# Optimization experiments

Hardware: AMD Instinct MI355X
Metric: run time of the kernel (lower is better)

The kernel has to match this reference:

```python
import jax, jax.numpy as jnp
import numpy as np

B, N, C = 2, 2048, 1024
H = 16
D = C // H
HID = 4 * C
EPS = 1e-5


def layernorm(x, g, b):
    mu = jnp.mean(x, axis=-1, keepdims=True)
    var = jnp.var(x, axis=-1, keepdims=True)
    return (x - mu) * jax.lax.rsqrt(var + EPS) * g + b


def setup_inputs() -> dict:
    key = jax.random.key(0)
    ks = jax.random.split(key, 8)
    s = lambda fan_in: 1.0 / np.sqrt(fan_in)
    return {
        "x": jax.random.normal(ks[0], (B, N, C), dtype=jnp.float32),
        "ln1_g": jnp.ones((C,), jnp.float32),
        "ln1_b": jnp.zeros((C,), jnp.float32),
        "w_qkv": jax.random.normal(ks[1], (C, 3 * C), jnp.float32) * s(C),
        "w_proj": jax.random.normal(ks[2], (C, C), jnp.float32) * s(C),
        "b_proj": jnp.zeros((C,), jnp.float32),
        "ln2_g": jnp.ones((C,), jnp.float32),
        "ln2_b": jnp.zeros((C,), jnp.float32),
        "w_fc1": jax.random.normal(ks[3], (C, HID), jnp.float32) * s(C),
        "b_fc1": jnp.zeros((HID,), jnp.float32),
        "w_fc2": jax.random.normal(ks[4], (HID, C), jnp.float32) * s(HID),
        "b_fc2": jnp.zeros((C,), jnp.float32),
        "metadata": 0,
        "thw_shape": 2048,
    }


def reference(x, ln1_g, ln1_b, w_qkv, w_proj, b_proj, ln2_g, ln2_b,
              w_fc1, b_fc1, w_fc2, b_fc2, metadata, thw_shape):
    scale = 1.0 / np.sqrt(D)
    # --- attention branch (pre-norm) ---
    xn = layernorm(x, ln1_g, ln1_b)
    qkv = (xn @ w_qkv).reshape(B, N, 3, H, D)
    q = jnp.transpose(qkv[:, :, 0], (0, 2, 1, 3))  # [B,H,N,D]
    k = jnp.transpose(qkv[:, :, 1], (0, 2, 1, 3))
    v = jnp.transpose(qkv[:, :, 2], (0, 2, 1, 3))
    attn = jax.nn.softmax(jnp.einsum('bhnd,bhmd->bhnm', q, k) * scale, axis=-1)
    o = jnp.einsum('bhnm,bhmd->bhnd', attn, v)
    o = jnp.transpose(o, (0, 2, 1, 3)).reshape(B, N, C)
    x = x + (o @ w_proj + b_proj)
    # --- MLP branch (pre-norm) ---
    xn2 = layernorm(x, ln2_g, ln2_b)
    h = jax.nn.gelu(xn2 @ w_fc1 + b_fc1, approximate=False)  # torch GELU = exact erf
    x = x + (h @ w_fc2 + b_fc2)
    return x
```

## Files before the change

kernel.cpp:

```cpp
#include <hip/hip_runtime.h>

#define B_   2
#define N_   2048
#define C_   1024
#define H_   16
#define D_   64
#define HID_ 4096
#define M_   (B_ * N_)

typedef __attribute__((ext_vector_type(8))) short bf16x8;
typedef __attribute__((ext_vector_type(4))) short short4v;
typedef __attribute__((ext_vector_type(4))) float f32x4;

__device__ __forceinline__ unsigned short f2bf(float f) {
  unsigned int u = __builtin_bit_cast(unsigned int, f);
  u += 0x7fffu + ((u >> 16) & 1u);
  return (unsigned short)(u >> 16);
}

__device__ __forceinline__ void gl2lds16(const void* g, void* l) {
  __builtin_amdgcn_global_load_lds(
      (const __attribute__((address_space(1))) unsigned int*)g,
      (__attribute__((address_space(3))) unsigned int*)l, 16, 0, 0);
}

__global__ __launch_bounds__(256) void ln_kernel(const float* __restrict__ x,
                                                 const float* __restrict__ g,
                                                 const float* __restrict__ bta,
                                                 unsigned short* __restrict__ out) {
  int row  = blockIdx.x * 4 + (threadIdx.x >> 6);
  int lane = threadIdx.x & 63;
  const float* xr = x + (size_t)row * C_;
  float4 v[4];
  float s1 = 0.f, s2 = 0.f;
#pragma unroll
  for (int j = 0; j < 4; j++) {
    v[j] = *(const float4*)(xr + j * 256 + lane * 4);
    s1 += v[j].x + v[j].y + v[j].z + v[j].w;
    s2 += v[j].x * v[j].x + v[j].y * v[j].y + v[j].z * v[j].z + v[j].w * v[j].w;
  }
#pragma unroll
  for (int m = 1; m < 64; m <<= 1) { s1 += __shfl_xor(s1, m); s2 += __shfl_xor(s2, m); }
  float mu  = s1 * (1.0f / C_);
  float var = s2 * (1.0f / C_) - mu * mu;
  float rs  = rsqrtf(var + 1e-5f);
#pragma unroll
  for (int j = 0; j < 4; j++) {
    const float4 gv = *(const float4*)(g + j * 256 + lane * 4);
    const float4 bv = *(const float4*)(bta + j * 256 + lane * 4);
    ushort4 o;
    o.x = f2bf((v[j].x - mu) * rs * gv.x + bv.x);
    o.y = f2bf((v[j].y - mu) * rs * gv.y + bv.y);
    o.z = f2bf((v[j].z - mu) * rs * gv.z + bv.z);
    o.w = f2bf((v[j].w - mu) * rs * gv.w + bv.w);
    *(ushort4*)(out + (size_t)row * C_ + j * 256 + lane * 4) = o;
  }
}

__global__ __launch_bounds__(256) void wtrans_kernel(const float* __restrict__ W,
                                                     unsigned short* __restrict__ Wt,
                                                     int K, int N) {
  __shared__ float t[32][33];
  int n0 = blockIdx.x * 32, k0 = blockIdx.y * 32;
  int tx = threadIdx.x, ty = threadIdx.y;
#pragma unroll
  for (int j = 0; j < 4; j++)
    t[ty + j * 8][tx] = W[(size_t)(k0 + ty + j * 8) * N + n0 + tx];
  __syncthreads();
#pragma unroll
  for (int j = 0; j < 4; j++)
    Wt[(size_t)(n0 + ty + j * 8) * K + k0 + tx] = f2bf(t[tx][ty + j * 8]);
}

__global__ __launch_bounds__(256) void vtrans_kernel(const unsigned short* __restrict__ v,
                                                     unsigned short* __restrict__ vt) {
  __shared__ unsigned short t[32][33];
  int bh = blockIdx.z;
  int n0 = blockIdx.x * 32, d0 = blockIdx.y * 32;
  const unsigned short* src = v + (size_t)bh * N_ * D_;
  unsigned short* dst = vt + (size_t)bh * D_ * N_;
  int tx = threadIdx.x, ty = threadIdx.y;
#pragma unroll
  for (int j = 0; j < 4; j++)
    t[ty + j * 8][tx] = src[(size_t)(n0 + ty + j * 8) * D_ + d0 + tx];
  __syncthreads();
#pragma unroll
  for (int j = 0; j < 4; j++)
    dst[(size_t)(d0 + ty + j * 8) * N_ + n0 + tx] = t[tx][ty + j * 8];
}

template <int MODE, int BN>
__global__ __launch_bounds__(256) void gemm_kernel(
    const unsigned short* __restrict__ A,
    const unsigned short* __restrict__ Wt,
    const float* __restrict__ bias,
    const float* __restrict__ resid,
    float* __restrict__ outf,
    unsigned short* __restrict__ outb0,
    unsigned short* __restrict__ outb1,
    unsigned short* __restrict__ outb2,
    int M, int N, int K) {
  constexpr int MT = (BN == 128) ? 4 : 2;
  __shared__ __align__(16) short As[128][64];
  __shared__ __align__(16) short Bs[BN][64];
  int tid = threadIdx.x;
  int w = tid >> 6, lane = tid & 63, r = lane & 15, quad = lane >> 4;
  int rowbase = (BN == 128) ? (w >> 1) * 64 : w * 32;
  int colbase = (BN == 128) ? (w & 1) * 64 : 0;
  int bM = blockIdx.y * 128, bN = blockIdx.x * BN;

  int srow   = (w << 3) + (lane >> 3);
  int schunk = (lane & 7) ^ ((lane >> 3) & 7);
  const unsigned short* aP = A  + (size_t)(bM + srow) * K + schunk * 8;
  const unsigned short* bP = Wt + (size_t)(bN + srow) * K + schunk * 8;

  int pc0 = (quad ^ (r & 7)) * 8;

  f32x4 acc[MT][4];
#pragma unroll
  for (int i = 0; i < MT; i++)
#pragma unroll
    for (int j = 0; j < 4; j++) acc[i][j] = f32x4{0.f, 0.f, 0.f, 0.f};

  for (int k0 = 0; k0 < K; k0 += 64) {
    __syncthreads();
#pragma unroll
    for (int p = 0; p < 4; p++)
      gl2lds16(aP + (size_t)(p * 32) * K + k0, &As[p * 32 + (w << 3)][0]);
#pragma unroll
    for (int p = 0; p < BN / 32; p++)
      gl2lds16(bP + (size_t)(p * 32) * K + k0, &Bs[p * 32 + (w << 3)][0]);
    __syncthreads();
#pragma unroll
    for (int kh = 0; kh < 2; kh++) {
      int pc = pc0 ^ (kh * 32);
      bf16x8 af[MT], bfr[4];
#pragma unroll
      for (int mt = 0; mt < MT; mt++)
        af[mt] = *(const bf16x8*)&As[rowbase + mt * 16 + r][pc];
#pragma unroll
      for (int nt = 0; nt < 4; nt++)
        bfr[nt] = *(const bf16x8*)&Bs[colbase + nt * 16 + r][pc];
#pragma unroll
      for (int mt = 0; mt < MT; mt++)
#pragma unroll
        for (int nt = 0; nt < 4; nt++)
          acc[mt][nt] = __builtin_amdgcn_mfma_f32_16x16x32_bf16(af[mt], bfr[nt], acc[mt][nt], 0, 0, 0);
    }
  }

#pragma unroll
  for (int mt = 0; mt < MT; mt++) {
#pragma unroll
    for (int nt = 0; nt < 4; nt++) {
#pragma unroll
      for (int i = 0; i < 4; i++) {
        int gm = bM + rowbase + mt * 16 + quad * 4 + i;
        int gn = bN + colbase + nt * 16 + r;
        float val = acc[mt][nt][i];
        if (MODE == 0) {
          int s = gn >> 10, c = gn & 1023;
          int hh = c >> 6, d = c & 63;
          int b = gm >> 11, n = gm & 2047;
          size_t di = ((size_t)(b * H_ + hh) * N_ + n) * D_ + d;
          unsigned short bvv = f2bf(s == 0 ? val * 0.125f : val);
          (s == 0 ? outb0 : (s == 1 ? outb1 : outb2))[di] = bvv;
        } else if (MODE == 1) {
          outf[(size_t)gm * N + gn] = val + bias[gn] + resid[(size_t)gm * N + gn];
        } else {
          float t = val + bias[gn];
          float gl = 0.5f * t * (1.0f + erff(t * 0.70710678118f));
          outb0[(size_t)gm * N + gn] = f2bf(gl);
        }
      }
    }
  }
}

template <int MODE>
__global__ __launch_bounds__(512, 2) void gemm256_kernel(
    const unsigned short* __restrict__ A,
    const unsigned short* __restrict__ Wt,
    const float* __restrict__ bias,
    float* __restrict__ outf,
    const float* __restrict__ resid,
    unsigned short* __restrict__ outb0,
    unsigned short* __restrict__ outb1,
    unsigned short* __restrict__ outb2,
    int M, int N, int K) {
  __shared__ __align__(16) short As[2][256][64];
  __shared__ __align__(16) short Bs[2][256][64];
  const int tid = threadIdx.x;
  const int w = tid >> 6, lane = tid & 63, r = lane & 15, quad = lane >> 4;
  const int wr = w >> 2, wc = w & 3;
  const int bN = blockIdx.x * 256, bM = blockIdx.y * 256;

  const int srow   = (w << 3) + (lane >> 3);
  const int schunk = (lane & 7) ^ ((lane >> 3) & 7);
  const unsigned short* aSrc = A  + (size_t)(bM + srow) * K + schunk * 8;
  const unsigned short* bSrc = Wt + (size_t)(bN + srow) * K + schunk * 8;
  const int wrow = w << 3;

  const int ntiles = K >> 6;
  const int tmask  = ntiles - 1;

#define STAGE_H(t, h)                                                            \
  do {                                                                           \
    int b_ = (t) & 1, tt_ = (t) & tmask;                                         \
    if ((h) < 2) {                                                               \
      const unsigned short* p_ = aSrc + (size_t)((h) * 128) * K + tt_ * 64;      \
      gl2lds16(p_, &As[b_][(h) * 128 + wrow][0]);                                \
      gl2lds16(p_ + (size_t)64 * K, &As[b_][(h) * 128 + 64 + wrow][0]);          \
    } else {                                                                     \
      const unsigned short* p_ = bSrc + (size_t)(((h) - 2) * 128) * K + tt_ * 64;\
      gl2lds16(p_, &Bs[b_][((h) - 2) * 128 + wrow][0]);                          \
      gl2lds16(p_ + (size_t)64 * K, &Bs[b_][((h) - 2) * 128 + 64 + wrow][0]);    \
    }                                                                            \
  } while (0)

  f32x4 acc[8][4];
#pragma unroll
  for (int i = 0; i < 8; i++)
#pragma unroll
    for (int j = 0; j < 4; j++) acc[i][j] = f32x4{0.f, 0.f, 0.f, 0.f};

  bf16x8 af[4][2];
  bf16x8 bfr[4][2];

#define RD_A(b, msub)                                                            \
  {                                                                              \
    _Pragma("unroll") for (int mt_ = 0; mt_ < 4; mt_++)                          \
      _Pragma("unroll") for (int ks_ = 0; ks_ < 2; ks_++)                        \
        af[mt_][ks_] = *(const bf16x8*)&As[b][wr * 128 + (msub) * 64 + mt_ * 16 + r] \
                                          [((ks_ * 4 + quad) ^ (r & 7)) * 8];    \
  }
#define RD_B(b, nh)                                                              \
  {                                                                              \
    _Pragma("unroll") for (int nt_ = 0; nt_ < 2; nt_++)                          \
      _Pragma("unroll") for (int ks_ = 0; ks_ < 2; ks_++)                        \
        bfr[(nh) * 2 + nt_][ks_] =                                               \
            *(const bf16x8*)&Bs[b][wc * 64 + (nh) * 32 + nt_ * 16 + r]           \
                               [((ks_ * 4 + quad) ^ (r & 7)) * 8];               \
  }
#define MM_Q(msub, nh)                                                           \
  {                                                                              \
    _Pragma("unroll") for (int mt_ = 0; mt_ < 4; mt_++)                          \
      _Pragma("unroll") for (int nt_ = 0; nt_ < 2; nt_++)                        \
        _Pragma("unroll") for (int ks_ = 0; ks_ < 2; ks_++)                      \
          acc[(msub) * 4 + mt_][(nh) * 2 + nt_] =                                \
              __builtin_amdgcn_mfma_f32_16x16x32_bf16(                           \
                  af[mt_][ks_], bfr[(nh) * 2 + nt_][ks_],                        \
                  acc[(msub) * 4 + mt_][(nh) * 2 + nt_], 0, 0, 0);               \
  }

#define BARRIER() asm volatile("s_barrier" ::: "memory")
#define WAITL()   asm volatile("s_waitcnt lgkmcnt(0)" ::: "memory")
#define WAITV2()  asm volatile("s_waitcnt vmcnt(2)" ::: "memory")
#define PRIO1()   __builtin_amdgcn_s_setprio(1)
#define PRIO0()   __builtin_amdgcn_s_setprio(0)

  STAGE_H(0, 0); STAGE_H(0, 1); STAGE_H(0, 2); STAGE_H(0, 3);
  STAGE_H(1, 0);
  WAITV2();
  BARRIER();

  const int niter = ntiles >> 1;
  for (int i = 0; i < niter; i++) {
    const int tc = 2 * i;
    RD_A(0, 0); RD_B(0, 0);
    STAGE_H(tc + 1, 1);
    BARRIER(); WAITL();
    PRIO1(); MM_Q(0, 0); PRIO0();
    BARRIER();
    RD_B(0, 1);
    STAGE_H(tc + 1, 2);
    BARRIER(); WAITL();
    PRIO1(); MM_Q(0, 1); PRIO0();
    BARRIER();
    RD_A(0, 1);
    STAGE_H(tc + 1, 3);
    BARRIER(); WAITL();
    PRIO1(); MM_Q(1, 1); PRIO0();
    BARRIER();
    STAGE_H(tc + 2, 0);
    BARRIER(); WAITL();
    PRIO1(); MM_Q(1, 0); PRIO0();
    WAITV2();
    BARRIER();
    RD_A(1, 0); RD_B(1, 0);
    STAGE_H(tc + 2, 1);
    BARRIER(); WAITL();
    PRIO1(); MM_Q(0, 0); PRIO0();
    BARRIER();
    RD_B(1, 1);
    STAGE_H(tc + 2, 2);
    BARRIER(); WAITL();
    PRIO1(); MM_Q(0, 1); PRIO0();
    BARRIER();
    RD_A(1, 1);
    STAGE_H(tc + 2, 3);
    BARRIER(); WAITL();
    PRIO1(); MM_Q(1, 1); PRIO0();
    BARRIER();
    STAGE_H(tc + 3, 0);
    BARRIER(); WAITL();
    PRIO1(); MM_Q(1, 0); PRIO0();
    WAITV2();
    BARRIER();
  }

#pragma unroll
  for (int m = 0; m < 8; m++) {
#pragma unroll
    for (int n = 0; n < 4; n++) {
#pragma unroll
      for (int i2 = 0; i2 < 4; i2++) {
        int gm = bM + wr * 128 + m * 16 + quad * 4 + i2;
        int gn = bN + wc * 64 + n * 16 + r;
        float val = acc[m][n][i2];
        if (MODE == 0) {
          int s = gn >> 10, c = gn & 1023;
          int hh = c >> 6, d = c & 63;
          int b = gm >> 11, nn = gm & 2047;
          size_t di = ((size_t)(b * H_ + hh) * N_ + nn) * D_ + d;
          unsigned short bvv = f2bf(s == 0 ? val * 0.125f : val);
          (s == 0 ? outb0 : (s == 1 ? outb1 : outb2))[di] = bvv;
        } else if (MODE == 1) {
          outf[(size_t)gm * N + gn] = val + bias[gn] + resid[(size_t)gm * N + gn];
        } else {
          float t = val + bias[gn];
          float gl = 0.5f * t * (1.0f + erff(t * 0.70710678118f));
          outb0[(size_t)gm * N + gn] = f2bf(gl);
        }
      }
    }
  }
#undef STAGE_H
#undef RD_A
#undef RD_B
#undef MM_Q
#undef BARRIER
#undef WAITL
#undef WAITV2
#undef PRIO1
#undef PRIO0
}

__global__ __launch_bounds__(256) void attn_kernel(const unsigned short* __restrict__ qb,
                                                   const unsigned short* __restrict__ kb,
                                                   const unsigned short* __restrict__ vtb,
                                                   unsigned short* __restrict__ ob) {
  __shared__ __align__(16) short Ks[128][64];
  __shared__ __align__(16) short Vts[64][128];
  int tid = threadIdx.x;
  int w = tid >> 6, lane = tid & 63, r = lane & 15, quad = lane >> 4;
  int bh = blockIdx.x >> 4, qt = blockIdx.x & 15;
  const unsigned short* qh  = qb  + (size_t)bh * N_ * D_;
  const unsigned short* kh  = kb  + (size_t)bh * N_ * D_;
  const unsigned short* vth = vtb + (size_t)bh * D_ * N_;

  bf16x8 qf[2][2];
#pragma unroll
  for (int mt = 0; mt < 2; mt++)
#pragma unroll
    for (int ks = 0; ks < 2; ks++)
      qf[mt][ks] = *(const bf16x8*)(qh + (size_t)(qt * 128 + w * 32 + mt * 16 + r) * D_ + ks * 32 + quad * 8);

  float mst[2] = {-1e30f, -1e30f}, lst[2] = {0.f, 0.f};
  f32x4 oacc[2][4];
#pragma unroll
  for (int mt = 0; mt < 2; mt++)
#pragma unroll
    for (int nt = 0; nt < 4; nt++) oacc[mt][nt] = f32x4{0.f, 0.f, 0.f, 0.f};

  int krow   = (w << 3) + (lane >> 3);
  int kchunk = (lane & 7) ^ ((lane >> 3) & 7);
  const unsigned short* kP = kh + (size_t)krow * D_ + kchunk * 8;
  int vrow   = (w << 2) + (lane >> 4);
  int vchunk = (lane & 15) ^ (vrow & 7);
  const unsigned short* vP = vth + (size_t)vrow * N_ + vchunk * 8;

  short* Plw = &Ks[0][0] + w * 2048;
  int swz = (r & 7);

  for (int t = 0; t < 16; t++) {
    __syncthreads();
#pragma unroll
    for (int p = 0; p < 4; p++)
      gl2lds16(kP + (size_t)(t * 128 + p * 32) * D_, &Ks[p * 32 + (w << 3)][0]);
#pragma unroll
    for (int p = 0; p < 4; p++)
      gl2lds16(vP + (size_t)(p * 16) * N_ + t * 128, &Vts[p * 16 + (w << 2)][0]);
    __syncthreads();

    f32x4 sacc[2][8];
#pragma unroll
    for (int mt = 0; mt < 2; mt++)
#pragma unroll
      for (int nt = 0; nt < 8; nt++) sacc[mt][nt] = f32x4{0.f, 0.f, 0.f, 0.f};
#pragma unroll
    for (int ks = 0; ks < 2; ks++) {
#pragma unroll
      for (int nt = 0; nt < 8; nt++) {
        bf16x8 kfr = *(const bf16x8*)&Ks[nt * 16 + r][((ks * 4 + quad) ^ swz) * 8];
#pragma unroll
        for (int mt = 0; mt < 2; mt++)
          sacc[mt][nt] = __builtin_amdgcn_mfma_f32_16x16x32_bf16(kfr, qf[mt][ks], sacc[mt][nt], 0, 0, 0);
      }
    }

    float alpha[2];
#pragma unroll
    for (int mt = 0; mt < 2; mt++) {
      float tm = -1e30f;
#pragma unroll
      for (int nt = 0; nt < 8; nt++)
#pragma unroll
        for (int i = 0; i < 4; i++) tm = fmaxf(tm, sacc[mt][nt][i]);
      tm = fmaxf(tm, __shfl_xor(tm, 16));
      tm = fmaxf(tm, __shfl_xor(tm, 32));
      float mnew = fmaxf(mst[mt], tm);
      alpha[mt] = __expf(mst[mt] - mnew);
      mst[mt] = mnew;
      float rs = 0.f;
#pragma unroll
      for (int nt = 0; nt < 8; nt++)
#pragma unroll
        for (int i = 0; i < 4; i++) {
          float p = __expf(sacc[mt][nt][i] - mnew);
          sacc[mt][nt][i] = p;
          rs += p;
        }
      rs += __shfl_xor(rs, 16);
      rs += __shfl_xor(rs, 32);
      lst[mt] = lst[mt] * alpha[mt] + rs;
#pragma unroll
      for (int i = 0; i < 4; i++) {
        float av = __shfl(alpha[mt], (lane & 48) | (quad * 4 + i));
#pragma unroll
        for (int nt = 0; nt < 4; nt++) oacc[mt][nt][i] *= av;
      }
    }

    __syncthreads();

#pragma unroll
    for (int mt = 0; mt < 2; mt++) {
#pragma unroll
      for (int nt = 0; nt < 8; nt++) {
        short4v pk;
        pk[0] = (short)f2bf(sacc[mt][nt][0]);
        pk[1] = (short)f2bf(sacc[mt][nt][1]);
        pk[2] = (short)f2bf(sacc[mt][nt][2]);
        pk[3] = (short)f2bf(sacc[mt][nt][3]);
        *(short4v*)&Plw[r * 128 + (((nt * 2 + (quad >> 1)) ^ swz) * 8) + (quad & 1) * 4] = pk;
      }
      asm volatile("" ::: "memory");
#pragma unroll
      for (int ks = 0; ks < 4; ks++) {
        bf16x8 pfr = *(const bf16x8*)&Plw[r * 128 + ((ks * 4 + quad) ^ swz) * 8];
#pragma unroll
        for (int nt2 = 0; nt2 < 4; nt2++) {
          bf16x8 vfr = *(const bf16x8*)&Vts[nt2 * 16 + r][((ks * 4 + quad) ^ swz) * 8];
          oacc[mt][nt2] = __builtin_amdgcn_mfma_f32_16x16x32_bf16(pfr, vfr, oacc[mt][nt2], 0, 0, 0);
        }
      }
      asm volatile("" ::: "memory");
    }
  }

  int bb = bh >> 4, hh = bh & 15;
#pragma unroll
  for (int mt = 0; mt < 2; mt++) {
#pragma unroll
    for (int i = 0; i < 4; i++) {
      float li = __shfl(lst[mt], (lane & 48) | (quad * 4 + i));
      float inv = 1.0f / li;
      int row = qt * 128 + w * 32 + mt * 16 + quad * 4 + i;
#pragma unroll
      for (int nt2 = 0; nt2 < 4; nt2++) {
        int d = nt2 * 16 + r;
        ob[((size_t)bb * N_ + row) * C_ + hh * D_ + d] = f2bf(oacc[mt][nt2][i] * inv);
      }
    }
  }
}

extern "C" void kernel_launch(void* const* d_in, const int* in_sizes, int n_in,
                              void* d_out, int out_size, void* d_ws, size_t ws_size,
                              hipStream_t stream) {
  const float* x     = (const float*)d_in[0];
  const float* ln1g  = (const float*)d_in[1];
  const float* ln1b  = (const float*)d_in[2];
  const float* wqkv  = (const float*)d_in[3];
  const float* wproj = (const float*)d_in[4];
  const float* bproj = (const float*)d_in[5];
  const float* ln2g  = (const float*)d_in[6];
  const float* ln2b  = (const float*)d_in[7];
  const float* wfc1  = (const float*)d_in[8];
  const float* bfc1  = (const float*)d_in[9];
  const float* wfc2  = (const float*)d_in[10];
  const float* bfc2  = (const float*)d_in[11];
  float* out = (float*)d_out;

  const size_t MB = 1u << 20;
  if (ws_size < 88 * MB) return;
  char* w = (char*)d_ws;
  unsigned short* xn    = (unsigned short*)(w + 0 * MB);
  unsigned short* qbuf  = (unsigned short*)(w + 8 * MB);
  unsigned short* kbuf  = (unsigned short*)(w + 16 * MB);
  unsigned short* vbuf  = (unsigned short*)(w + 24 * MB);
  unsigned short* hbuf  = (unsigned short*)(w + 0 * MB);
  unsigned short* obuf  = (unsigned short*)(w + 32 * MB);
  float*          x2    = (float*)         (w + 40 * MB);
  unsigned short* xn2   = (unsigned short*)(w + 56 * MB);
  unsigned short* vtb   = (unsigned short*)(w + 56 * MB);
  unsigned short* wqkvt = (unsigned short*)(w + 64 * MB);
  unsigned short* wprjt = (unsigned short*)(w + 70 * MB);
  unsigned short* wfc1t = (unsigned short*)(w + 72 * MB);
  unsigned short* wfc2t = (unsigned short*)(w + 80 * MB);

  dim3 tb(32, 8);
  ln_kernel<<<M_ / 4, 256, 0, stream>>>(x, ln1g, ln1b, xn);
  wtrans_kernel<<<dim3(3 * C_ / 32, C_ / 32), tb, 0, stream>>>(wqkv, wqkvt, C_, 3 * C_);
  wtrans_kernel<<<dim3(C_ / 32, C_ / 32), tb, 0, stream>>>(wproj, wprjt, C_, C_);
  wtrans_kernel<<<dim3(HID_ / 32, C_ / 32), tb, 0, stream>>>(wfc1, wfc1t, C_, HID_);
  wtrans_kernel<<<dim3(C_ / 32, HID_ / 32), tb, 0, stream>>>(wfc2, wfc2t, HID_, C_);

  gemm256_kernel<0><<<dim3(3 * C_ / 256, M_ / 256), 512, 0, stream>>>(
      xn, wqkvt, nullptr, nullptr, nullptr, qbuf, kbuf, vbuf, M_, 3 * C_, C_);
  vtrans_kernel<<<dim3(N_ / 32, D_ / 32, B_ * H_), tb, 0, stream>>>(vbuf, vtb);
  attn_kernel<<<B_ * H_ * (N_ / 128), 256, 0, stream>>>(qbuf, kbuf, vtb, obuf);
  gemm_kernel<1, 64><<<dim3(C_ / 64, M_ / 128), 256, 0, stream>>>(
      obuf, wprjt, bproj, x, x2, nullptr, nullptr, nullptr, M_, C_, C_);
  ln_kernel<<<M_ / 4, 256, 0, stream>>>(x2, ln2g, ln2b, xn2);
  gemm256_kernel<2><<<dim3(HID_ / 256, M_ / 256), 512, 0, stream>>>(
      xn2, wfc1t, bfc1, nullptr, nullptr, hbuf, nullptr, nullptr, M_, HID_, C_);
  gemm_kernel<1, 64><<<dim3(C_ / 64, M_ / 128), 256, 0, stream>>>(
      hbuf, wfc2t, bfc2, x2, out, nullptr, nullptr, nullptr, M_, C_, HID_);
}
```

Before: 384.9 us.

## Double-buffer attention K/V, fuse V transpose into QKV epilogue, batch weight transposes

Measured after the change: 355.2 us. 7.7% less time.

```diff
diff --git a/kernel.cpp b/kernel.cpp
--- a/kernel.cpp
+++ b/kernel.cpp
@@ -9,7 +9,6 @@
 #define M_   (B_ * N_)
 
 typedef __attribute__((ext_vector_type(8))) short bf16x8;
-typedef __attribute__((ext_vector_type(4))) short short4v;
 typedef __attribute__((ext_vector_type(4))) float f32x4;
 
 __device__ __forceinline__ unsigned short f2bf(float f) {
@@ -18,11 +17,25 @@
   return (unsigned short)(u >> 16);
 }
 
+__device__ __forceinline__ unsigned int cvtpk(float a, float b) {
+  unsigned int r;
+  asm("v_cvt_pk_bf16_f32 %0, %1, %2" : "=v"(r) : "v"(a), "v"(b));
+  return r;
+}
+
+__device__ __forceinline__ float exp2a(float x) {
+  float r;
+  asm("v_exp_f32 %0, %1" : "=v"(r) : "v"(x));
+  return r;
+}
+
 __device__ __forceinline__ void gl2lds16(const void* g, void* l) {
   __builtin_amdgcn_global_load_lds(
       (const __attribute__((address_space(1))) unsigned int*)g,
       (__attribute__((address_space(3))) unsigned int*)l, 16, 0, 0);
 }
+
+#define LOG2E 1.44269504088896f
 
 __global__ __launch_bounds__(256) void ln_kernel(const float* __restrict__ x,
                                                  const float* __restrict__ g,
@@ -57,11 +70,20 @@
   }
 }
 
-__global__ __launch_bounds__(256) void wtrans_kernel(const float* __restrict__ W,
-                                                     unsigned short* __restrict__ Wt,
-                                                     int K, int N) {
+__global__ __launch_bounds__(256) void wtrans_all(
+    const float* __restrict__ w0, const float* __restrict__ w1,
+    const float* __restrict__ w2, const float* __restrict__ w3,
+    unsigned short* __restrict__ o0, unsigned short* __restrict__ o1,
+    unsigned short* __restrict__ o2, unsigned short* __restrict__ o3) {
+  int id = blockIdx.x;
+  const float* W; unsigned short* Wt; int K, N, rel;
+  if (id < 3072)      { W = w0; Wt = o0; K = 1024; N = 3072; rel = id; }
+  else if (id < 4096) { W = w1; Wt = o1; K = 1024; N = 1024; rel = id - 3072; }
+  else if (id < 8192) { W = w2; Wt = o2; K = 1024; N = 4096; rel = id - 4096; }
+  else                { W = w3; Wt = o3; K = 4096; N = 1024; rel = id - 8192; }
+  int nx = N >> 5;
+  int n0 = (rel % nx) * 32, k0 = (rel / nx) * 32;
   __shared__ float t[32][33];
-  int n0 = blockIdx.x * 32, k0 = blockIdx.y * 32;
   int tx = threadIdx.x, ty = threadIdx.y;
 #pragma unroll
   for (int j = 0; j < 4; j++)
@@ -70,23 +92,6 @@
 #pragma unroll
   for (int j = 0; j < 4; j++)
     Wt[(size_t)(n0 + ty + j * 8) * K + k0 + tx] = f2bf(t[tx][ty + j * 8]);
-}
-
-__global__ __launch_bounds__(256) void vtrans_kernel(const unsigned short* __restrict__ v,
-                                                     unsigned short* __restrict__ vt) {
-  __shared__ unsigned short t[32][33];
-  int bh = blockIdx.z;
-  int n0 = blockIdx.x * 32, d0 = blockIdx.y * 32;
-  const unsigned short* src = v + (size_t)bh * N_ * D_;
-  unsigned short* dst = vt + (size_t)bh * D_ * N_;
-  int tx = threadIdx.x, ty = threadIdx.y;
-#pragma unroll
-  for (int j = 0; j < 4; j++)
-    t[ty + j * 8][tx] = src[(size_t)(n0 + ty + j * 8) * D_ + d0 + tx];
-  __syncthreads();
-#pragma unroll
-  for (int j = 0; j < 4; j++)
-    dst[(size_t)(d0 + ty + j * 8) * N_ + n0 + tx] = t[tx][ty + j * 8];
 }
 
 template <int MODE, int BN>
@@ -97,8 +102,6 @@
     const float* __restrict__ resid,
     float* __restrict__ outf,
     unsigned short* __restrict__ outb0,
-    unsigned short* __restrict__ outb1,
-    unsigned short* __restrict__ outb2,
     int M, int N, int K) {
   constexpr int MT = (BN == 128) ? 4 : 2;
   __shared__ __align__(16) short As[128][64];
@@ -158,14 +161,7 @@
         int gm = bM + rowbase + mt * 16 + quad * 4 + i;
         int gn = bN + colbase + nt * 16 + r;
         float val = acc[mt][nt][i];
-        if (MODE == 0) {
-          int s = gn >> 10, c = gn & 1023;
-          int hh = c >> 6, d = c & 63;
-          int b = gm >> 11, n = gm & 2047;
-          size_t di = ((size_t)(b * H_ + hh) * N_ + n) * D_ + d;
-          unsigned short bvv = f2bf(s == 0 ? val * 0.125f : val);
-          (s == 0 ? outb0 : (s == 1 ? outb1 : outb2))[di] = bvv;
-        } else if (MODE == 1) {
+        if (MODE == 1) {
           outf[(size_t)gm * N + gn] = val + bias[gn] + resid[(size_t)gm * N + gn];
         } else {
           float t = val + bias[gn];
@@ -182,8 +178,6 @@
     const unsigned short* __restrict__ A,
     const unsigned short* __restrict__ Wt,
     const float* __restrict__ bias,
-    float* __restrict__ outf,
-    const float* __restrict__ resid,
     unsigned short* __restrict__ outb0,
     unsigned short* __restrict__ outb1,
     unsigned short* __restrict__ outb2,
@@ -313,24 +307,31 @@
   for (int m = 0; m < 8; m++) {
 #pragma unroll
     for (int n = 0; n < 4; n++) {
-#pragma unroll
-      for (int i2 = 0; i2 < 4; i2++) {
-        int gm = bM + wr * 128 + m * 16 + quad * 4 + i2;
-        int gn = bN + wc * 64 + n * 16 + r;
-        float val = acc[m][n][i2];
-        if (MODE == 0) {
-          int s = gn >> 10, c = gn & 1023;
-          int hh = c >> 6, d = c & 63;
-          int b = gm >> 11, nn = gm & 2047;
-          size_t di = ((size_t)(b * H_ + hh) * N_ + nn) * D_ + d;
-          unsigned short bvv = f2bf(s == 0 ? val * 0.125f : val);
-          (s == 0 ? outb0 : (s == 1 ? outb1 : outb2))[di] = bvv;
-        } else if (MODE == 1) {
-          outf[(size_t)gm * N + gn] = val + bias[gn] + resid[(size_t)gm * N + gn];
+      int gm0 = bM + wr * 128 + m * 16 + quad * 4;
+      int gn  = bN + wc * 64 + n * 16 + r;
+      if (MODE == 0) {
+        int s = gn >> 10, c = gn & 1023;
+        int hh = c >> 6, d = c & 63;
+        int b = gm0 >> 11, n0 = gm0 & 2047;
+        if (s == 2) {
+          unsigned int p0 = cvtpk(acc[m][n][0], acc[m][n][1]);
+          unsigned int p1 = cvtpk(acc[m][n][2], acc[m][n][3]);
+          *(uint2*)(outb2 + ((size_t)(b * H_ + hh) * D_ + d) * N_ + n0) = uint2{p0, p1};
         } else {
-          float t = val + bias[gn];
+          unsigned short* dst = (s == 0) ? outb0 : outb1;
+          float sc = (s == 0) ? 0.125f * LOG2E : 1.0f;
+#pragma unroll
+          for (int i2 = 0; i2 < 4; i2++) {
+            size_t di = ((size_t)(b * H_ + hh) * N_ + n0 + i2) * D_ + d;
+            dst[di] = f2bf(acc[m][n][i2] * sc);
+          }
+        }
+      } else {
+#pragma unroll
+        for (int i2 = 0; i2 < 4; i2++) {
+          float t = acc[m][n][i2] + bias[gn];
           float gl = 0.5f * t * (1.0f + erff(t * 0.70710678118f));
-          outb0[(size_t)gm * N + gn] = f2bf(gl);
+          outb0[(size_t)(gm0 + i2) * N + gn] = f2bf(gl);
         }
       }
     }
@@ -346,25 +347,27 @@
 #undef PRIO0
 }
 
-__global__ __launch_bounds__(256) void attn_kernel(const unsigned short* __restrict__ qb,
-                                                   const unsigned short* __restrict__ kb,
-                                                   const unsigned short* __restrict__ vtb,
-                                                   unsigned short* __restrict__ ob) {
-  __shared__ __align__(16) short Ks[128][64];
-  __shared__ __align__(16) short Vts[64][128];
+__global__ __launch_bounds__(512, 2) void attn_kernel(const unsigned short* __restrict__ qb,
+                                                      const unsigned short* __restrict__ kb,
+                                                      const unsigned short* __restrict__ vtb,
+                                                      unsigned short* __restrict__ ob) {
+  __shared__ __align__(16) short Ks[2][128][64];
+  __shared__ __align__(16) short Vts[2][64][128];
+  __shared__ __align__(16) short Pl[8 * 16 * 128];
   int tid = threadIdx.x;
   int w = tid >> 6, lane = tid & 63, r = lane & 15, quad = lane >> 4;
-  int bh = blockIdx.x >> 4, qt = blockIdx.x & 15;
+  int bh = blockIdx.x & 31, qt = blockIdx.x >> 5;
   const unsigned short* qh  = qb  + (size_t)bh * N_ * D_;
   const unsigned short* kh  = kb  + (size_t)bh * N_ * D_;
   const unsigned short* vth = vtb + (size_t)bh * D_ * N_;
+  int swz = r & 7;
 
   bf16x8 qf[2][2];
 #pragma unroll
   for (int mt = 0; mt < 2; mt++)
 #pragma unroll
     for (int ks = 0; ks < 2; ks++)
-      qf[mt][ks] = *(const bf16x8*)(qh + (size_t)(qt * 128 + w * 32 + mt * 16 + r) * D_ + ks * 32 + quad * 8);
+      qf[mt][ks] = *(const bf16x8*)(qh + (size_t)(qt * 256 + w * 32 + mt * 16 + r) * D_ + ks * 32 + quad * 8);
 
   float mst[2] = {-1e30f, -1e30f}, lst[2] = {0.f, 0.f};
   f32x4 oacc[2][4];
@@ -373,25 +376,26 @@
 #pragma unroll
     for (int nt = 0; nt < 4; nt++) oacc[mt][nt] = f32x4{0.f, 0.f, 0.f, 0.f};
 
-  int krow   = (w << 3) + (lane >> 3);
-  int kchunk = (lane & 7) ^ ((lane >> 3) & 7);
-  const unsigned short* kP = kh + (size_t)krow * D_ + kchunk * 8;
-  int vrow   = (w << 2) + (lane >> 4);
-  int vchunk = (lane & 15) ^ (vrow & 7);
-  const unsigned short* vP = vth + (size_t)vrow * N_ + vchunk * 8;
-
-  short* Plw = &Ks[0][0] + w * 2048;
-  int swz = (r & 7);
+  const unsigned short* kBase = kh + (size_t)(tid >> 3) * D_ + ((tid & 7) ^ ((tid >> 3) & 7)) * 8;
+  const unsigned short* vBase = vth + (size_t)(tid >> 4) * N_ + ((tid & 15) ^ ((tid >> 4) & 7)) * 8;
+
+  short* Plw = &Pl[0] + w * 2048;
+
+  gl2lds16(kBase,                        &Ks[0][(w << 3)][0]);
+  gl2lds16(kBase + (size_t)64 * D_,      &Ks[0][64 + (w << 3)][0]);
+  gl2lds16(vBase,                        &Vts[0][(w << 2)][0]);
+  gl2lds16(vBase + (size_t)32 * N_,      &Vts[0][32 + (w << 2)][0]);
+  __syncthreads();
 
   for (int t = 0; t < 16; t++) {
-    __syncthreads();
-#pragma unroll
-    for (int p = 0; p < 4; p++)
-      gl2lds16(kP + (size_t)(t * 128 + p * 32) * D_, &Ks[p * 32 + (w << 3)][0]);
-#pragma unroll
-    for (int p = 0; p < 4; p++)
-      gl2lds16(vP + (size_t)(p * 16) * N_ + t * 128, &Vts[p * 16 + (w << 2)][0]);
-    __syncthreads();
+    const int cur = t & 1;
+    if (t < 15) {
+      const int nb = cur ^ 1;
+      gl2lds16(kBase + (size_t)(t + 1) * 128 * D_,                  &Ks[nb][(w << 3)][0]);
+      gl2lds16(kBase + (size_t)((t + 1) * 128 + 64) * D_,           &Ks[nb][64 + (w << 3)][0]);
+      gl2lds16(vBase + (size_t)(t + 1) * 128,                       &Vts[nb][(w << 2)][0]);
+      gl2lds16(vBase + (size_t)(t + 1) * 128 + (size_t)32 * N_,     &Vts[nb][32 + (w << 2)][0]);
+    }
 
     f32x4 sacc[2][8];
 #pragma unroll
@@ -402,14 +406,20 @@
     for (int ks = 0; ks < 2; ks++) {
 #pragma unroll
       for (int nt = 0; nt < 8; nt++) {
-        bf16x8 kfr = *(const bf16x8*)&Ks[nt * 16 + r][((ks * 4 + quad) ^ swz) * 8];
+        bf16x8 kfr = *(const bf16x8*)&Ks[cur][nt * 16 + r][((ks * 4 + quad) ^ swz) * 8];
 #pragma unroll
         for (int mt = 0; mt < 2; mt++)
           sacc[mt][nt] = __builtin_amdgcn_mfma_f32_16x16x32_bf16(kfr, qf[mt][ks], sacc[mt][nt], 0, 0, 0);
       }
     }
 
-    float alpha[2];
+    bf16x8 vfr[4][4];
+#pragma unroll
+    for (int ks = 0; ks < 4; ks++)
+#pragma unroll
+      for (int nt2 = 0; nt2 < 4; nt2++)
+        vfr[ks][nt2] = *(const bf16x8*)&Vts[cur][nt2 * 16 + r][((ks * 4 + quad) ^ swz) * 8];
+
 #pragma unroll
     for (int mt = 0; mt < 2; mt++) {
       float tm = -1e30f;
@@ -419,54 +429,54 @@
         for (int i = 0; i < 4; i++) tm = fmaxf(tm, sacc[mt][nt][i]);
       tm = fmaxf(tm, __shfl_xor(tm, 16));
       tm = fmaxf(tm, __shfl_xor(tm, 32));
-      float mnew = fmaxf(mst[mt], tm);
-      alpha[mt] = __expf(mst[mt] - mnew);
-      mst[mt] = mnew;
+      if (__ballot(tm > mst[mt] + 8.0f)) {
+        float mnew = fmaxf(mst[mt], tm);
+        float alpha = exp2a(mst[mt] - mnew);
+        mst[mt] = mnew;
+        lst[mt] *= alpha;
+#pragma unroll
+        for (int i = 0; i < 4; i++) {
+          float av = __shfl(alpha, (lane & 48) | (quad * 4 + i));
+#pragma unroll
+          for (int nt2 = 0; nt2 < 4; nt2++) oacc[mt][nt2][i] *= av;
+        }
+      }
+      float m = mst[mt];
       float rs = 0.f;
 #pragma unroll
       for (int nt = 0; nt < 8; nt++)
 #pragma unroll
         for (int i = 0; i < 4; i++) {
-          float p = __expf(sacc[mt][nt][i] - mnew);
+          float p = exp2a(sacc[mt][nt][i] - m);
           sacc[mt][nt][i] = p;
           rs += p;
         }
       rs += __shfl_xor(rs, 16);
       rs += __shfl_xor(rs, 32);
-      lst[mt] = lst[mt] * alpha[mt] + rs;
-#pragma unroll
-      for (int i = 0; i < 4; i++) {
-        float av = __shfl(alpha[mt], (lane & 48) | (quad * 4 + i));
-#pragma unroll
-        for (int nt = 0; nt < 4; nt++) oacc[mt][nt][i] *= av;
-      }
-    }
-
-    __syncthreads();
+      lst[mt] += rs;
+    }
 
 #pragma unroll
     for (int mt = 0; mt < 2; mt++) {
 #pragma unroll
       for (int nt = 0; nt < 8; nt++) {
-        short4v pk;
-        pk[0] = (short)f2bf(sacc[mt][nt][0]);
-        pk[1] = (short)f2bf(sacc[mt][nt][1]);
-        pk[2] = (short)f2bf(sacc[mt][nt][2]);
-        pk[3] = (short)f2bf(sacc[mt][nt][3]);
-        *(short4v*)&Plw[r * 128 + (((nt * 2 + (quad >> 1)) ^ swz) * 8) + (quad & 1) * 4] = pk;
+        uint2 pw;
+        pw.x = cvtpk(sacc[mt][nt][0], sacc[mt][nt][1]);
+        pw.y = cvtpk(sacc[mt][nt][2], sacc[mt][nt][3]);
+        *(uint2*)&Plw[r * 128 + (((nt * 2 + (quad >> 1)) ^ swz) * 8) + (quad & 1) * 4] = pw;
       }
       asm volatile("" ::: "memory");
 #pragma unroll
       for (int ks = 0; ks < 4; ks++) {
         bf16x8 pfr = *(const bf16x8*)&Plw[r * 128 + ((ks * 4 + quad) ^ swz) * 8];
 #pragma unroll
-        for (int nt2 = 0; nt2 < 4; nt2++) {
-          bf16x8 vfr = *(const bf16x8*)&Vts[nt2 * 16 + r][((ks * 4 + quad) ^ swz) * 8];
-          oacc[mt][nt2] = __builtin_amdgcn_mfma_f32_16x16x32_bf16(pfr, vfr, oacc[mt][nt2], 0, 0, 0);
-        }
+        for (int nt2 = 0; nt2 < 4; nt2++)
+          oacc[mt][nt2] = __builtin_amdgcn_mfma_f32_16x16x32_bf16(pfr, vfr[ks][nt2], oacc[mt][nt2], 0, 0, 0);
       }
       asm volatile("" ::: "memory");
     }
+
+    __syncthreads();
   }
 
   int bb = bh >> 4, hh = bh & 15;
@@ -476,7 +486,7 @@
     for (int i = 0; i < 4; i++) {
       float li = __shfl(lst[mt], (lane & 48) | (quad * 4 + i));
       float inv = 1.0f / li;
-      int row = qt * 128 + w * 32 + mt * 16 + quad * 4 + i;
+      int row = qt * 256 + w * 32 + mt * 16 + quad * 4 + i;
 #pragma unroll
       for (int nt2 = 0; nt2 < 4; nt2++) {
         int d = nt2 * 16 + r;
@@ -509,7 +519,6 @@
   unsigned short* xn    = (unsigned short*)(w + 0 * MB);
   unsigned short* qbuf  = (unsigned short*)(w + 8 * MB);
   unsigned short* kbuf  = (unsigned short*)(w + 16 * MB);
-  unsigned short* vbuf  = (unsigned short*)(w + 24 * MB);
   unsigned short* hbuf  = (unsigned short*)(w + 0 * MB);
   unsigned short* obuf  = (unsigned short*)(w + 32 * MB);
   float*          x2    = (float*)         (w + 40 * MB);
@@ -520,22 +529,18 @@
   unsigned short* wfc1t = (unsigned short*)(w + 72 * MB);
   unsigned short* wfc2t = (unsigned short*)(w + 80 * MB);
 
-  dim3 tb(32, 8);
   ln_kernel<<<M_ / 4, 256, 0, stream>>>(x, ln1g, ln1b, xn);
-  wtrans_kernel<<<dim3(3 * C_ / 32, C_ / 32), tb, 0, stream>>>(wqkv, wqkvt, C_, 3 * C_);
-  wtrans_kernel<<<dim3(C_ / 32, C_ / 32), tb, 0, stream>>>(wproj, wprjt, C_, C_);
-  wtrans_kernel<<<dim3(HID_ / 32, C_ / 32), tb, 0, stream>>>(wfc1, wfc1t, C_, HID_);
-  wtrans_kernel<<<dim3(C_ / 32, HID_ / 32), tb, 0, stream>>>(wfc2, wfc2t, HID_, C_);
+  wtrans_all<<<12288, dim3(32, 8), 0, stream>>>(wqkv, wproj, wfc1, wfc2,
+                                                wqkvt, wprjt, wfc1t, wfc2t);
 
   gemm256_kernel<0><<<dim3(3 * C_ / 256, M_ / 256), 512, 0, stream>>>(
-      xn, wqkvt, nullptr, nullptr, nullptr, qbuf, kbuf, vbuf, M_, 3 * C_, C_);
-  vtrans_kernel<<<dim3(N_ / 32, D_ / 32, B_ * H_), tb, 0, stream>>>(vbuf, vtb);
-  attn_kernel<<<B_ * H_ * (N_ / 128), 256, 0, stream>>>(qbuf, kbuf, vtb, obuf);
+      xn, wqkvt, nullptr, qbuf, kbuf, vtb, M_, 3 * C_, C_);
+  attn_kernel<<<B_ * H_ * (N_ / 256), 512, 0, stream>>>(qbuf, kbuf, vtb, obuf);
   gemm_kernel<1, 64><<<dim3(C_ / 64, M_ / 128), 256, 0, stream>>>(
-      obuf, wprjt, bproj, x, x2, nullptr, nullptr, nullptr, M_, C_, C_);
+      obuf, wprjt, bproj, x, x2, nullptr, M_, C_, C_);
   ln_kernel<<<M_ / 4, 256, 0, stream>>>(x2, ln2g, ln2b, xn2);
   gemm256_kernel<2><<<dim3(HID_ / 256, M_ / 256), 512, 0, stream>>>(
-      xn2, wfc1t, bfc1, nullptr, nullptr, hbuf, nullptr, nullptr, M_, HID_, C_);
+      xn2, wfc1t, bfc1, hbuf, nullptr, nullptr, M_, HID_, C_);
   gemm_kernel<1, 64><<<dim3(C_ / 64, M_ / 128), 256, 0, stream>>>(
-      hbuf, wfc2t, bfc2, x2, out, nullptr, nullptr, nullptr, M_, C_, HID_);
-}
+      hbuf, wfc2t, bfc2, x2, out, nullptr, M_, C_, HID_);
+}
```
